# Kernel optimization log

Measured on AMD Instinct MI355X. Metric: run time of the kernel, lower is better.

The kernel has to match this reference:

```python
import jax, jax.numpy as jnp
import numpy as np

B, L, C, D = 32, 256, 16, 128
WORD_VOCAB, CHR_VOCAB = 50000, 128


def conv1d(x, w, b):
    # x: [N, D, T], w: [D_out, D_in, 3], torch Conv1d (cross-correlation), padding=1
    y = jax.lax.conv_general_dilated(x, w, window_strides=(1,), padding=[(1, 1)],
                                     dimension_numbers=('NCH', 'OIH', 'NCH'))
    return y + b[None, :, None]


def setup_inputs() -> dict:
    key = jax.random.key(0)
    k1, k2, k3, k4, k5, k6, k7, k8 = jax.random.split(key, 8)
    word_vector = jax.random.randint(k1, (B, L), 0, WORD_VOCAB)
    words_in_char = jax.random.randint(k2, (B, L, C), 0, CHR_VOCAB)
    # embedding tables, padding_idx=0 -> row 0 is zeros
    word_table = (jax.random.normal(k3, (WORD_VOCAB, D), jnp.float32) * 0.02).at[0].set(0.0)
    chr_table = (jax.random.normal(k4, (CHR_VOCAB, D), jnp.float32) * 0.02).at[0].set(0.0)
    scale = 1.0 / np.sqrt(D * 3)
    conv_chr_w = jax.random.normal(k5, (D, D, 3), jnp.float32) * scale
    conv_chr_b = jax.random.normal(k6, (D,), jnp.float32) * scale
    conv_word_w = jax.random.normal(k7, (D, D, 3), jnp.float32) * scale
    conv_word_b = jax.random.normal(k8, (D,), jnp.float32) * scale
    return dict(word_vector=word_vector, words_in_char=words_in_char,
                word_table=word_table, chr_table=chr_table,
                conv_chr_w=conv_chr_w, conv_chr_b=conv_chr_b,
                conv_word_w=conv_word_w, conv_word_b=conv_word_b)


def reference(word_vector, words_in_char, word_table, chr_table,
              conv_chr_w, conv_chr_b, conv_word_w, conv_word_b):
    # --- char path (batched version of the per-word Python loop) ---
    chr_emb = chr_table[words_in_char]                       # [B, L, C, D]
    x = chr_emb.reshape(B * L, C, D).transpose(0, 2, 1)      # [B*L, D, C]
    word_conv = conv1d(x, conv_chr_w, conv_chr_b)            # [B*L, D, C]
    char_feats = word_conv.max(axis=2).reshape(B, L, D)      # max over char positions
    # --- word path ---
    word_emb = word_table[word_vector]                       # [B, L, D]
    out = conv1d(word_emb.transpose(0, 2, 1), conv_word_w, conv_word_b)  # [B, D, L]
    # stack both branch outputs into one array: [2, B, D, L]
    return jnp.stack([out, char_feats.transpose(0, 2, 1)])
```

## Files before the change

### kernel.cpp

```cpp
#include <hip/hip_runtime.h>

typedef __attribute__((ext_vector_type(8))) short short8;
typedef __attribute__((ext_vector_type(4))) float float4_t;

#define NB 32
#define NL 256
#define ND 128
#define OUT_PLANE (NB * ND * NL)
#define XS 136
#define FR_WORD 49152
#define CHRB 98304

__device__ inline unsigned short f2bf(float f) {
    union { float f; unsigned int i; } c;
    c.f = f;
    unsigned int r = c.i + 0x7FFFu + ((c.i >> 16) & 1u);
    return (unsigned short)(r >> 16);
}

__global__ void make_frags(const float* __restrict__ Wc,
                           const float* __restrict__ Ww,
                           const float* __restrict__ chrT,
                           unsigned short* __restrict__ out) {
    int i = blockIdx.x * 256 + threadIdx.x;
    if (i < CHRB) {
        const float* W = (i < FR_WORD) ? Wc : Ww;
        int ii = (i < FR_WORD) ? i : i - FR_WORD;
        int j    = ii & 7;
        int lane = (ii >> 3) & 63;
        int nt   = (ii >> 9) & 7;
        int s    = ii >> 12;
        int dout = nt * 16 + (lane & 15);
        int t    = s >> 2;
        int k    = (s & 3) * 32 + ((lane >> 4) & 3) * 8 + j;
        out[i] = f2bf(W[(dout * 128 + k) * 3 + t]);
    } else {
        int j = i - CHRB;
        out[i] = f2bf(chrT[j]);
    }
}

__global__ __launch_bounds__(128, 2) void conv_kernel(
    const int* __restrict__ wv, const int* __restrict__ wic,
    const float* __restrict__ wordT,
    const unsigned short* __restrict__ ws,
    const float* __restrict__ biasC, const float* __restrict__ biasW,
    float* __restrict__ out) {
    __shared__ unsigned short X[18 * XS];
    const int tid  = threadIdx.x;
    const int wave = tid >> 6, lane = tid & 63;
    const int m = lane & 15, quad = lane >> 4;
    const int bid = blockIdx.x;

    if (bid >= 512) {
        const unsigned short* chrB = ws + CHRB;
        const int w0 = (bid - 512) * 8;
        short8 bfrag[12][4];
#pragma unroll
        for (int s = 0; s < 12; ++s)
#pragma unroll
            for (int p = 0; p < 4; ++p)
                bfrag[s][p] = *(const short8*)(
                    ws + (((s * 8 + wave * 4 + p) * 64 + lane) << 3));
        float bb[4];
#pragma unroll
        for (int p = 0; p < 4; ++p) bb[p] = biasC[wave * 64 + p * 16 + m];

        int base = w0 * 16 + m;
        int i0 = (m >= 1)  ? wic[base - 1] : 0;
        int i1 = wic[base];
        int i2 = (m < 15) ? wic[base + 1] : 0;

#pragma unroll
        for (int wl = 0; wl < 8; ++wl) {
            const int w = w0 + wl;
            const unsigned short* r0 = chrB + i0 * 128 + (quad << 3);
            const unsigned short* r1 = chrB + i1 * 128 + (quad << 3);
            const unsigned short* r2 = chrB + i2 * 128 + (quad << 3);
            short8 A[4];
            A[0] = *(const short8*)(r0);
            A[1] = *(const short8*)(r0 + 32);
            A[2] = *(const short8*)(r0 + 64);
            A[3] = *(const short8*)(r0 + 96);

            if (wl < 7) {
                int nb = (w + 1) * 16 + m;
                i0 = (m >= 1)  ? wic[nb - 1] : 0;
                i1 = wic[nb];
                i2 = (m < 15) ? wic[nb + 1] : 0;
            }

            float4_t acc[4];
#pragma unroll
            for (int p = 0; p < 4; ++p) acc[p] = (float4_t){0.f, 0.f, 0.f, 0.f};

#pragma unroll
            for (int s = 0; s < 4; ++s) {
                short8 a = A[s];
                A[s] = *(const short8*)(r1 + (s << 5));
#pragma unroll
                for (int p = 0; p < 4; ++p)
                    acc[p] = __builtin_amdgcn_mfma_f32_16x16x32_bf16(
                        a, bfrag[s][p], acc[p], 0, 0, 0);
            }
#pragma unroll
            for (int s = 0; s < 4; ++s) {
                short8 a = A[s];
                A[s] = *(const short8*)(r2 + (s << 5));
#pragma unroll
                for (int p = 0; p < 4; ++p)
                    acc[p] = __builtin_amdgcn_mfma_f32_16x16x32_bf16(
                        a, bfrag[s + 4][p], acc[p], 0, 0, 0);
            }
#pragma unroll
            for (int s = 0; s < 4; ++s) {
#pragma unroll
                for (int p = 0; p < 4; ++p)
                    acc[p] = __builtin_amdgcn_mfma_f32_16x16x32_bf16(
                        A[s], bfrag[s + 8][p], acc[p], 0, 0, 0);
            }

            int b = w >> 8, l = w & 255;
            float* obase = out + OUT_PLANE + b * (ND * NL) + l;
#pragma unroll
            for (int p = 0; p < 4; ++p) {
                float v = fmaxf(fmaxf(acc[p].x, acc[p].y),
                                fmaxf(acc[p].z, acc[p].w));
                v = fmaxf(v, __shfl_xor(v, 16, 64));
                v = fmaxf(v, __shfl_xor(v, 32, 64));
                v += bb[p];
                if (quad == 0) obase[(wave * 64 + p * 16 + m) * NL] = v;
            }
        }
    } else {
        const int b = bid >> 4, l0 = (bid & 15) << 4;
        short8 bfrag[12][4];
#pragma unroll
        for (int s = 0; s < 12; ++s)
#pragma unroll
            for (int p = 0; p < 4; ++p)
                bfrag[s][p] = *(const short8*)(
                    ws + FR_WORD + (((s * 8 + wave * 4 + p) * 64 + lane) << 3));
        float bb[4];
#pragma unroll
        for (int p = 0; p < 4; ++p) bb[p] = biasW[wave * 64 + p * 16 + m];

#pragma unroll
        for (int i0 = 0; i0 < 2; ++i0) {
            int i = tid + i0 * 128;
            if (i < 144) {
                int rr = i >> 3, sg = i & 7;
                int l = l0 + rr - 1;
                int idx = (l >= 0 && l < NL) ? wv[b * NL + l] : 0;
                const float4_t* src =
                    (const float4_t*)(wordT + idx * 128 + sg * 16);
                float4_t f0 = src[0], f1 = src[1], f2 = src[2], f3 = src[3];
                unsigned short t16[16];
                t16[0]=f2bf(f0.x); t16[1]=f2bf(f0.y); t16[2]=f2bf(f0.z); t16[3]=f2bf(f0.w);
                t16[4]=f2bf(f1.x); t16[5]=f2bf(f1.y); t16[6]=f2bf(f1.z); t16[7]=f2bf(f1.w);
                t16[8]=f2bf(f2.x); t16[9]=f2bf(f2.y); t16[10]=f2bf(f2.z); t16[11]=f2bf(f2.w);
                t16[12]=f2bf(f3.x); t16[13]=f2bf(f3.y); t16[14]=f2bf(f3.z); t16[15]=f2bf(f3.w);
                *(short8*)&X[rr * XS + sg * 16]     = *(const short8*)&t16[0];
                *(short8*)&X[rr * XS + sg * 16 + 8] = *(const short8*)&t16[8];
            }
        }
        __syncthreads();

        float4_t acc[4];
#pragma unroll
        for (int p = 0; p < 4; ++p) acc[p] = (float4_t){0.f, 0.f, 0.f, 0.f};
#pragma unroll
        for (int s = 0; s < 12; ++s) {
            short8 a = *(const short8*)&X[(m + (s >> 2)) * XS +
                                          (s & 3) * 32 + quad * 8];
#pragma unroll
            for (int p = 0; p < 4; ++p)
                acc[p] = __builtin_amdgcn_mfma_f32_16x16x32_bf16(
                    a, bfrag[s][p], acc[p], 0, 0, 0);
        }

        float* obase = out + b * (ND * NL) + l0 + quad * 4;
#pragma unroll
        for (int p = 0; p < 4; ++p) {
            int dout = wave * 64 + p * 16 + m;
            float4_t pk;
            pk.x = acc[p].x + bb[p];
            pk.y = acc[p].y + bb[p];
            pk.z = acc[p].z + bb[p];
            pk.w = acc[p].w + bb[p];
            *(float4_t*)&obase[dout * NL] = pk;
        }
    }
}

extern "C" void kernel_launch(void* const* d_in, const int* in_sizes, int n_in,
                              void* d_out, int out_size, void* d_ws,
                              size_t ws_size, hipStream_t stream) {
    const int* word_vector   = (const int*)d_in[0];
    const int* words_in_char = (const int*)d_in[1];
    const float* word_table  = (const float*)d_in[2];
    const float* chr_table   = (const float*)d_in[3];
    const float* conv_chr_w  = (const float*)d_in[4];
    const float* conv_chr_b  = (const float*)d_in[5];
    const float* conv_word_w = (const float*)d_in[6];
    const float* conv_word_b = (const float*)d_in[7];
    float* out            = (float*)d_out;
    unsigned short* wsp   = (unsigned short*)d_ws;

    make_frags<<<448, 256, 0, stream>>>(conv_chr_w, conv_word_w, chr_table, wsp);
    conv_kernel<<<1536, 128, 0, stream>>>(word_vector, words_in_char,
                                          word_table, wsp,
                                          conv_chr_b, conv_word_b, out);
}
```

Before: 117.8 us.

## Stage char embeddings in double-buffered LDS and batch char-path output stores

The char path no longer has each lane gather its three shifted embedding rows straight from global memory. The block now cooperatively gathers each word's 16 char rows once into a zero-padded shared-memory tile, double-buffered so the next word's gather overlaps the current word's MFMAs. The shifted A operands for all 12 MFMA steps are read from LDS. Max-pooled results for four consecutive words are held in registers and written as one float4, replacing scalar strided stores. This adds a __syncthreads per word and doubles the shared buffer, which may reduce occupancy.

```diff
diff --git a/kernel.cpp b/kernel.cpp
--- a/kernel.cpp
+++ b/kernel.cpp
@@ -46,7 +46,7 @@
     const unsigned short* __restrict__ ws,
     const float* __restrict__ biasC, const float* __restrict__ biasW,
     float* __restrict__ out) {
-    __shared__ unsigned short X[18 * XS];
+    __shared__ unsigned short X[2][18 * XS];
     const int tid  = threadIdx.x;
     const int wave = tid >> 6, lane = tid & 63;
     const int m = lane & 15, quad = lane >> 4;
@@ -55,6 +55,7 @@
     if (bid >= 512) {
         const unsigned short* chrB = ws + CHRB;
         const int w0 = (bid - 512) * 8;
+        const int b = w0 >> 8, l0 = w0 & 255;
         short8 bfrag[12][4];
 #pragma unroll
         for (int s = 0; s < 12; ++s)
@@ -66,70 +67,74 @@
 #pragma unroll
         for (int p = 0; p < 4; ++p) bb[p] = biasC[wave * 64 + p * 16 + m];
 
-        int base = w0 * 16 + m;
-        int i0 = (m >= 1)  ? wic[base - 1] : 0;
-        int i1 = wic[base];
-        int i2 = (m < 15) ? wic[base + 1] : 0;
-
+        for (int p = tid; p < XS; p += 128) {
+            X[0][p] = 0; X[0][17 * XS + p] = 0;
+            X[1][p] = 0; X[1][17 * XS + p] = 0;
+        }
+        const int ra = tid >> 4, sub = tid & 15;
+
+        {
+            int j0 = wic[w0 * 16 + ra];
+            int j1 = wic[w0 * 16 + ra + 8];
+            short8 g0 = *(const short8*)(chrB + j0 * 128 + sub * 8);
+            short8 g1 = *(const short8*)(chrB + j1 * 128 + sub * 8);
+            *(short8*)&X[0][(ra + 1) * XS + sub * 8] = g0;
+            *(short8*)&X[0][(ra + 9) * XS + sub * 8] = g1;
+        }
+        int iA0 = wic[(w0 + 1) * 16 + ra];
+        int iA1 = wic[(w0 + 1) * 16 + ra + 8];
+        __syncthreads();
+
+        float v[4][4];
 #pragma unroll
         for (int wl = 0; wl < 8; ++wl) {
-            const int w = w0 + wl;
-            const unsigned short* r0 = chrB + i0 * 128 + (quad << 3);
-            const unsigned short* r1 = chrB + i1 * 128 + (quad << 3);
-            const unsigned short* r2 = chrB + i2 * 128 + (quad << 3);
-            short8 A[4];
-            A[0] = *(const short8*)(r0);
-            A[1] = *(const short8*)(r0 + 32);
-            A[2] = *(const short8*)(r0 + 64);
-            A[3] = *(const short8*)(r0 + 96);
-
+            const int cur = wl & 1;
+            short8 g0, g1;
             if (wl < 7) {
-                int nb = (w + 1) * 16 + m;
-                i0 = (m >= 1)  ? wic[nb - 1] : 0;
-                i1 = wic[nb];
-                i2 = (m < 15) ? wic[nb + 1] : 0;
+                g0 = *(const short8*)(chrB + iA0 * 128 + sub * 8);
+                g1 = *(const short8*)(chrB + iA1 * 128 + sub * 8);
+            }
+            int iB0 = 0, iB1 = 0;
+            if (wl < 6) {
+                iB0 = wic[(w0 + wl + 2) * 16 + ra];
+                iB1 = wic[(w0 + wl + 2) * 16 + ra + 8];
             }
 
             float4_t acc[4];
 #pragma unroll
             for (int p = 0; p < 4; ++p) acc[p] = (float4_t){0.f, 0.f, 0.f, 0.f};
-
-#pragma unroll
-            for (int s = 0; s < 4; ++s) {
-                short8 a = A[s];
-                A[s] = *(const short8*)(r1 + (s << 5));
+#pragma unroll
+            for (int s = 0; s < 12; ++s) {
+                short8 a = *(const short8*)&X[cur][(m + (s >> 2)) * XS +
+                                                  (s & 3) * 32 + quad * 8];
 #pragma unroll
                 for (int p = 0; p < 4; ++p)
                     acc[p] = __builtin_amdgcn_mfma_f32_16x16x32_bf16(
                         a, bfrag[s][p], acc[p], 0, 0, 0);
             }
-#pragma unroll
-            for (int s = 0; s < 4; ++s) {
-                short8 a = A[s];
-                A[s] = *(const short8*)(r2 + (s << 5));
-#pragma unroll
-                for (int p = 0; p < 4; ++p)
-                    acc[p] = __builtin_amdgcn_mfma_f32_16x16x32_bf16(
-                        a, bfrag[s + 4][p], acc[p], 0, 0, 0);
-            }
-#pragma unroll
-            for (int s = 0; s < 4; ++s) {
-#pragma unroll
-                for (int p = 0; p < 4; ++p)
-                    acc[p] = __builtin_amdgcn_mfma_f32_16x16x32_bf16(
-                        A[s], bfrag[s + 8][p], acc[p], 0, 0, 0);
-            }
-
-            int b = w >> 8, l = w & 255;
-            float* obase = out + OUT_PLANE + b * (ND * NL) + l;
+
+            if (wl < 7) {
+                *(short8*)&X[cur ^ 1][(ra + 1) * XS + sub * 8] = g0;
+                *(short8*)&X[cur ^ 1][(ra + 9) * XS + sub * 8] = g1;
+                iA0 = iB0; iA1 = iB1;
+            }
+            __syncthreads();
+
 #pragma unroll
             for (int p = 0; p < 4; ++p) {
-                float v = fmaxf(fmaxf(acc[p].x, acc[p].y),
+                float t = fmaxf(fmaxf(acc[p].x, acc[p].y),
                                 fmaxf(acc[p].z, acc[p].w));
-                v = fmaxf(v, __shfl_xor(v, 16, 64));
-                v = fmaxf(v, __shfl_xor(v, 32, 64));
-                v += bb[p];
-                if (quad == 0) obase[(wave * 64 + p * 16 + m) * NL] = v;
+                t = fmaxf(t, __shfl_xor(t, 16, 64));
+                t = fmaxf(t, __shfl_xor(t, 32, 64));
+                v[p][wl & 3] = t + bb[p];
+            }
+            if ((wl & 3) == 3 && quad == 0) {
+                float* obase = out + OUT_PLANE + b * (ND * NL) + l0 + (wl & 4);
+#pragma unroll
+                for (int p = 0; p < 4; ++p) {
+                    float4_t pk = {v[p][0], v[p][1], v[p][2], v[p][3]};
+                    *(float4_t*)&obase[(wave * 64 + p * 16 + m) * NL] = pk;
+                }
             }
         }
     } else {
@@ -160,8 +165,8 @@
                 t16[4]=f2bf(f1.x); t16[5]=f2bf(f1.y); t16[6]=f2bf(f1.z); t16[7]=f2bf(f1.w);
                 t16[8]=f2bf(f2.x); t16[9]=f2bf(f2.y); t16[10]=f2bf(f2.z); t16[11]=f2bf(f2.w);
                 t16[12]=f2bf(f3.x); t16[13]=f2bf(f3.y); t16[14]=f2bf(f3.z); t16[15]=f2bf(f3.w);
-                *(short8*)&X[rr * XS + sg * 16]     = *(const short8*)&t16[0];
-                *(short8*)&X[rr * XS + sg * 16 + 8] = *(const short8*)&t16[8];
+                *(short8*)&X[0][rr * XS + sg * 16]     = *(const short8*)&t16[0];
+                *(short8*)&X[0][rr * XS + sg * 16 + 8] = *(const short8*)&t16[8];
             }
         }
         __syncthreads();
@@ -171,8 +176,8 @@
         for (int p = 0; p < 4; ++p) acc[p] = (float4_t){0.f, 0.f, 0.f, 0.f};
 #pragma unroll
         for (int s = 0; s < 12; ++s) {
-            short8 a = *(const short8*)&X[(m + (s >> 2)) * XS +
-                                          (s & 3) * 32 + quad * 8];
+            short8 a = *(const short8*)&X[0][(m + (s >> 2)) * XS +
+                                            (s & 3) * 32 + quad * 8];
 #pragma unroll
             for (int p = 0; p < 4; ++p)
                 acc[p] = __builtin_amdgcn_mfma_f32_16x16x32_bf16(
```

After: 107.6 us. 8.7% less time.

## Use single-wave blocks covering all output channels with LDS double-buffered char rows

Applied to the files above, without the earlier changes.

Blocks shrink from two waves to one, and each wave now computes all 128 output channels, holding 12x8 bf16 weight fragments in registers. The char path stages gathered embedding rows through double-buffered shared memory instead of loading shifted rows straight from global memory, and prefetches the next word's rows during the MFMAs. The aim is to gather each char row once per word rather than three times per wave, and to drop the inter-wave split. In exchange register pressure rises sharply (96 short8 fragments plus 8 accumulators) and blocks have half the threads, so occupancy and latency hiding may suffer. The single-wave LDS use relies on in-order wave execution rather than explicit barriers.

```diff
diff --git a/kernel.cpp b/kernel.cpp
--- a/kernel.cpp
+++ b/kernel.cpp
@@ -8,6 +8,7 @@
 #define ND 128
 #define OUT_PLANE (NB * ND * NL)
 #define XS 136
+#define BUFSZ (18 * XS)
 #define FR_WORD 49152
 #define CHRB 98304
 
@@ -40,155 +41,155 @@
     }
 }
 
-__global__ __launch_bounds__(128, 2) void conv_kernel(
+__global__ __launch_bounds__(64, 1) void conv_kernel(
     const int* __restrict__ wv, const int* __restrict__ wic,
     const float* __restrict__ wordT,
     const unsigned short* __restrict__ ws,
     const float* __restrict__ biasC, const float* __restrict__ biasW,
     float* __restrict__ out) {
-    __shared__ unsigned short X[18 * XS];
-    const int tid  = threadIdx.x;
-    const int wave = tid >> 6, lane = tid & 63;
+    __shared__ unsigned short Xs[2 * BUFSZ];
+    const int lane = threadIdx.x;
     const int m = lane & 15, quad = lane >> 4;
     const int bid = blockIdx.x;
 
     if (bid >= 512) {
         const unsigned short* chrB = ws + CHRB;
         const int w0 = (bid - 512) * 8;
-        short8 bfrag[12][4];
+        const int b = w0 >> 8;
+        short8 bfrag[12][8];
 #pragma unroll
         for (int s = 0; s < 12; ++s)
 #pragma unroll
-            for (int p = 0; p < 4; ++p)
+            for (int p = 0; p < 8; ++p)
                 bfrag[s][p] = *(const short8*)(
-                    ws + (((s * 8 + wave * 4 + p) * 64 + lane) << 3));
-        float bb[4];
-#pragma unroll
-        for (int p = 0; p < 4; ++p) bb[p] = biasC[wave * 64 + p * 16 + m];
-
-        int base = w0 * 16 + m;
-        int i0 = (m >= 1)  ? wic[base - 1] : 0;
-        int i1 = wic[base];
-        int i2 = (m < 15) ? wic[base + 1] : 0;
-
-#pragma unroll
-        for (int wl = 0; wl < 8; ++wl) {
-            const int w = w0 + wl;
-            const unsigned short* r0 = chrB + i0 * 128 + (quad << 3);
-            const unsigned short* r1 = chrB + i1 * 128 + (quad << 3);
-            const unsigned short* r2 = chrB + i2 * 128 + (quad << 3);
-            short8 A[4];
-            A[0] = *(const short8*)(r0);
-            A[1] = *(const short8*)(r0 + 32);
-            A[2] = *(const short8*)(r0 + 64);
-            A[3] = *(const short8*)(r0 + 96);
-
-            if (wl < 7) {
-                int nb = (w + 1) * 16 + m;
-                i0 = (m >= 1)  ? wic[nb - 1] : 0;
-                i1 = wic[nb];
-                i2 = (m < 15) ? wic[nb + 1] : 0;
-            }
-
-            float4_t acc[4];
-#pragma unroll
-            for (int p = 0; p < 4; ++p) acc[p] = (float4_t){0.f, 0.f, 0.f, 0.f};
-
-#pragma unroll
-            for (int s = 0; s < 4; ++s) {
-                short8 a = A[s];
-                A[s] = *(const short8*)(r1 + (s << 5));
-#pragma unroll
-                for (int p = 0; p < 4; ++p)
+                    ws + (((s * 8 + p) * 64 + lane) << 3));
+
+        for (int p = lane; p < XS; p += 64) {
+            Xs[p] = 0; Xs[17 * XS + p] = 0;
+            Xs[BUFSZ + p] = 0; Xs[BUFSZ + 17 * XS + p] = 0;
+        }
+
+        int nidx[4];
+        {
+            int cidx[4];
+#pragma unroll
+            for (int q = 0; q < 4; ++q) cidx[q] = wic[w0 * 16 + quad + 4 * q];
+            short8 g[4];
+#pragma unroll
+            for (int q = 0; q < 4; ++q)
+                g[q] = *(const short8*)(chrB + cidx[q] * 128 + m * 8);
+#pragma unroll
+            for (int q = 0; q < 4; ++q)
+                *(short8*)&Xs[(quad + 4 * q + 1) * XS + m * 8] = g[q];
+#pragma unroll
+            for (int q = 0; q < 4; ++q)
+                nidx[q] = wic[(w0 + 1) * 16 + quad + 4 * q];
+        }
+
+        for (int j = 0; j < 8; ++j) {
+            unsigned short* bufC = &Xs[(j & 1) * BUFSZ];
+            unsigned short* bufN = &Xs[((j + 1) & 1) * BUFSZ];
+
+            short8 g[4];
+            if (j < 7) {
+#pragma unroll
+                for (int q = 0; q < 4; ++q)
+                    g[q] = *(const short8*)(chrB + nidx[q] * 128 + m * 8);
+            }
+            int tindx[4];
+            if (j < 6) {
+#pragma unroll
+                for (int q = 0; q < 4; ++q)
+                    tindx[q] = wic[(w0 + j + 2) * 16 + quad + 4 * q];
+            }
+
+            float4_t acc[8];
+#pragma unroll
+            for (int p = 0; p < 8; ++p) acc[p] = (float4_t){0.f,0.f,0.f,0.f};
+#pragma unroll
+            for (int s = 0; s < 12; ++s) {
+                short8 a = *(const short8*)&bufC[(m + (s >> 2)) * XS +
+                                                 (s & 3) * 32 + quad * 8];
+#pragma unroll
+                for (int p = 0; p < 8; ++p)
                     acc[p] = __builtin_amdgcn_mfma_f32_16x16x32_bf16(
                         a, bfrag[s][p], acc[p], 0, 0, 0);
             }
-#pragma unroll
-            for (int s = 0; s < 4; ++s) {
-                short8 a = A[s];
-                A[s] = *(const short8*)(r2 + (s << 5));
-#pragma unroll
-                for (int p = 0; p < 4; ++p)
-                    acc[p] = __builtin_amdgcn_mfma_f32_16x16x32_bf16(
-                        a, bfrag[s + 4][p], acc[p], 0, 0, 0);
-            }
-#pragma unroll
-            for (int s = 0; s < 4; ++s) {
-#pragma unroll
-                for (int p = 0; p < 4; ++p)
-                    acc[p] = __builtin_amdgcn_mfma_f32_16x16x32_bf16(
-                        A[s], bfrag[s + 8][p], acc[p], 0, 0, 0);
-            }
-
-            int b = w >> 8, l = w & 255;
+
+            if (j < 7) {
+#pragma unroll
+                for (int q = 0; q < 4; ++q)
+                    *(short8*)&bufN[(quad + 4 * q + 1) * XS + m * 8] = g[q];
+                if (j < 6) {
+#pragma unroll
+                    for (int q = 0; q < 4; ++q) nidx[q] = tindx[q];
+                }
+            }
+
+            int l = (w0 + j) & 255;
             float* obase = out + OUT_PLANE + b * (ND * NL) + l;
 #pragma unroll
-            for (int p = 0; p < 4; ++p) {
+            for (int p = 0; p < 8; ++p) {
                 float v = fmaxf(fmaxf(acc[p].x, acc[p].y),
                                 fmaxf(acc[p].z, acc[p].w));
                 v = fmaxf(v, __shfl_xor(v, 16, 64));
                 v = fmaxf(v, __shfl_xor(v, 32, 64));
-                v += bb[p];
-                if (quad == 0) obase[(wave * 64 + p * 16 + m) * NL] = v;
+                if (quad == 0)
+                    obase[(p * 16 + m) * NL] = v + biasC[p * 16 + m];
             }
         }
     } else {
         const int b = bid >> 4, l0 = (bid & 15) << 4;
-        short8 bfrag[12][4];
+        short8 bfrag[12][8];
 #pragma unroll
         for (int s = 0; s < 12; ++s)
 #pragma unroll
-            for (int p = 0; p < 4; ++p)
+            for (int p = 0; p < 8; ++p)
                 bfrag[s][p] = *(const short8*)(
-                    ws + FR_WORD + (((s * 8 + wave * 4 + p) * 64 + lane) << 3));
-        float bb[4];
-#pragma unroll
-        for (int p = 0; p < 4; ++p) bb[p] = biasW[wave * 64 + p * 16 + m];
-
-#pragma unroll
-        for (int i0 = 0; i0 < 2; ++i0) {
-            int i = tid + i0 * 128;
-            if (i < 144) {
-                int rr = i >> 3, sg = i & 7;
-                int l = l0 + rr - 1;
+                    ws + FR_WORD + (((s * 8 + p) * 64 + lane) << 3));
+
+#pragma unroll
+        for (int q = 0; q < 5; ++q) {
+            int jj = lane + 64 * q;
+            if (jj < 288) {
+                int row = jj >> 4, sub = jj & 15;
+                int l = l0 + row - 1;
                 int idx = (l >= 0 && l < NL) ? wv[b * NL + l] : 0;
                 const float4_t* src =
-                    (const float4_t*)(wordT + idx * 128 + sg * 16);
-                float4_t f0 = src[0], f1 = src[1], f2 = src[2], f3 = src[3];
-                unsigned short t16[16];
-                t16[0]=f2bf(f0.x); t16[1]=f2bf(f0.y); t16[2]=f2bf(f0.z); t16[3]=f2bf(f0.w);
-                t16[4]=f2bf(f1.x); t16[5]=f2bf(f1.y); t16[6]=f2bf(f1.z); t16[7]=f2bf(f1.w);
-                t16[8]=f2bf(f2.x); t16[9]=f2bf(f2.y); t16[10]=f2bf(f2.z); t16[11]=f2bf(f2.w);
-                t16[12]=f2bf(f3.x); t16[13]=f2bf(f3.y); t16[14]=f2bf(f3.z); t16[15]=f2bf(f3.w);
-                *(short8*)&X[rr * XS + sg * 16]     = *(const short8*)&t16[0];
-                *(short8*)&X[rr * XS + sg * 16 + 8] = *(const short8*)&t16[8];
-            }
-        }
-        __syncthreads();
-
-        float4_t acc[4];
-#pragma unroll
-        for (int p = 0; p < 4; ++p) acc[p] = (float4_t){0.f, 0.f, 0.f, 0.f};
+                    (const float4_t*)(wordT + idx * 128 + sub * 8);
+                float4_t f0 = src[0], f1 = src[1];
+                unsigned short t16[8];
+                t16[0]=f2bf(f0.x); t16[1]=f2bf(f0.y);
+                t16[2]=f2bf(f0.z); t16[3]=f2bf(f0.w);
+                t16[4]=f2bf(f1.x); t16[5]=f2bf(f1.y);
+                t16[6]=f2bf(f1.z); t16[7]=f2bf(f1.w);
+                *(short8*)&Xs[row * XS + sub * 8] = *(const short8*)t16;
+            }
+        }
+
+        float4_t acc[8];
+#pragma unroll
+        for (int p = 0; p < 8; ++p) acc[p] = (float4_t){0.f,0.f,0.f,0.f};
 #pragma unroll
         for (int s = 0; s < 12; ++s) {
-            short8 a = *(const short8*)&X[(m + (s >> 2)) * XS +
-                                          (s & 3) * 32 + quad * 8];
-#pragma unroll
-            for (int p = 0; p < 4; ++p)
+            short8 a = *(const short8*)&Xs[(m + (s >> 2)) * XS +
+                                           (s & 3) * 32 + quad * 8];
+#pragma unroll
+            for (int p = 0; p < 8; ++p)
                 acc[p] = __builtin_amdgcn_mfma_f32_16x16x32_bf16(
                     a, bfrag[s][p], acc[p], 0, 0, 0);
         }
 
         float* obase = out + b * (ND * NL) + l0 + quad * 4;
 #pragma unroll
-        for (int p = 0; p < 4; ++p) {
-            int dout = wave * 64 + p * 16 + m;
+        for (int p = 0; p < 8; ++p) {
+            float bw = biasW[p * 16 + m];
             float4_t pk;
-            pk.x = acc[p].x + bb[p];
-            pk.y = acc[p].y + bb[p];
-            pk.z = acc[p].z + bb[p];
-            pk.w = acc[p].w + bb[p];
-            *(float4_t*)&obase[dout * NL] = pk;
+            pk.x = acc[p].x + bw;
+            pk.y = acc[p].y + bw;
+            pk.z = acc[p].z + bw;
+            pk.w = acc[p].w + bw;
+            *(float4_t*)&obase[(p * 16 + m) * NL] = pk;
         }
     }
 }
@@ -208,7 +209,7 @@
     unsigned short* wsp   = (unsigned short*)d_ws;
 
     make_frags<<<448, 256, 0, stream>>>(conv_chr_w, conv_word_w, chr_table, wsp);
-    conv_kernel<<<1536, 128, 0, stream>>>(word_vector, words_in_char,
-                                          word_table, wsp,
-                                          conv_chr_b, conv_word_b, out);
-}
+    conv_kernel<<<1536, 64, 0, stream>>>(word_vector, words_in_char,
+                                         word_table, wsp,
+                                         conv_chr_b, conv_word_b, out);
+}
```

Measured after the change: 119.3 us. About the same (+1.2%).
